# Kernel tuning notes

Hardware: AMD Instinct MI355X
Metric: run time of the kernel (lower is better)

Reference implementation:

```python
import jax, jax.numpy as jnp
import numpy as np

B, N, F_, H, K_IN, K = 2, 768, 128, 128, 2, 2
TAU = 0.66


def setup_inputs() -> dict:
    key = jax.random.key(0)
    ks = jax.random.split(key, 8)
    s = lambda fan: 1.0 / np.sqrt(fan)
    X = jax.random.normal(ks[0], (B, N, F_), jnp.float32)
    # edge_feat RezeroMLP: Linear(F,H) -> act -> Linear(H,H)
    ef_w1 = jax.random.normal(ks[1], (F_, H), jnp.float32) * s(F_)
    ef_b1 = jnp.zeros((H,), jnp.float32)
    ef_w2 = jax.random.normal(ks[2], (H, H), jnp.float32) * s(H)
    ef_b2 = jnp.zeros((H,), jnp.float32)
    # rezero gate (init 0 in module; use small nonzero so the branch is exercised)
    gate = jnp.asarray(0.1, jnp.float32)
    # score_mlp RezeroMLP: Linear(k_in,H) -> ReLU -> Linear(H,k)
    sm_w1 = jax.random.normal(ks[3], (K_IN, H), jnp.float32) * s(K_IN)
    sm_b1 = jnp.zeros((H,), jnp.float32)
    sm_w2 = jax.random.normal(ks[4], (H, K), jnp.float32) * s(H)
    sm_b2 = jnp.zeros((K,), jnp.float32)
    # pre-sampled standard Gumbel noise for gumbel_softmax
    u = jax.random.uniform(ks[5], (B, N, N, K), jnp.float32, minval=1e-6, maxval=1.0 - 1e-6)
    gumbel = -jnp.log(-jnp.log(u))
    return {"X": X, "ef_w1": ef_w1, "ef_b1": ef_b1, "ef_w2": ef_w2, "ef_b2": ef_b2,
            "gate": gate, "sm_w1": sm_w1, "sm_b1": sm_b1, "sm_w2": sm_w2, "sm_b2": sm_b2,
            "gumbel": gumbel}


def reference(X, ef_w1, ef_b1, ef_w2, ef_b2, gate, sm_w1, sm_b1, sm_w2, sm_b2, gumbel):
    # edge_feat MLP: [B,N,F] -> [B,N,H]
    feats = jax.nn.relu(X @ ef_w1 + ef_b1) @ ef_w2 + ef_b2
    D = H // K_IN
    Xact = feats.reshape(B, N, D, K_IN)
    Xskip = X.reshape(B, N, D, K_IN)  # feat_dim == hidden_dim, proj is None
    Xc = (Xskip + gate * Xact).transpose(0, 3, 1, 2)  # [B,k_in,N,D]
    # pairwise outer product ('prod' scoring): [B,N,N,k_in]
    prod = jnp.einsum('bkid,bkjd->bijk', Xc, Xc)
    # per-edge score MLP: k_in -> H -> k
    scores = jax.nn.relu(prod @ sm_w1 + sm_b1) @ sm_w2 + sm_b2  # [B,N,N,k]
    logits = scores - jnp.max(scores, axis=-1, keepdims=True)
    # gumbel-softmax, hard (straight-through)
    y_soft = jax.nn.softmax((logits + gumbel) / TAU, axis=-1)
    y_hard = jax.nn.one_hot(jnp.argmax(y_soft, axis=-1), K, dtype=y_soft.dtype)
    y = y_hard + y_soft - jax.lax.stop_gradient(y_soft)
    # A = y @ zo with zo = [0,1,...]: probability/one-hot mass of 'edge' states
    zo = jnp.ones((K,), y.dtype).at[0].set(0.0)
    A = y @ zo  # [B,N,N]
    # zero diagonal and symmetrize via upper triangle
    Au = jnp.triu(A, 1)
    return Au + jnp.swapaxes(Au, -1, -2)
```

## Files before the change

### kernel.cpp

```cpp
#include <hip/hip_runtime.h>

#define BB 2
#define NN 768
#define FF 128
#define HH 128
#define TS 32
#define LST 68
#define NT (NN / TS)
#define NPAIR (NT * (NT + 1) / 2)
#define EROWS 2
#define THR 4e-3f

__device__ __forceinline__
double edge_exact_f64(const double* __restrict__ Xc, const double* __restrict__ wpack,
                      int b, int i, int j, double init) {
    const double* xi0 = Xc + ((size_t)(b * 2 + 0) * NN + i) * 64;
    const double* xj0 = Xc + ((size_t)(b * 2 + 0) * NN + j) * 64;
    const double* xi1 = Xc + ((size_t)(b * 2 + 1) * NN + i) * 64;
    const double* xj1 = Xc + ((size_t)(b * 2 + 1) * NN + j) * 64;
    double p0 = 0.0, p1 = 0.0;
#pragma unroll 4
    for (int d2 = 0; d2 < 32; ++d2) {
        double2 a0 = *(const double2*)&xi0[2 * d2];
        double2 b0 = *(const double2*)&xj0[2 * d2];
        double2 a1 = *(const double2*)&xi1[2 * d2];
        double2 b1 = *(const double2*)&xj1[2 * d2];
        p0 = fma(a0.y, b0.y, fma(a0.x, b0.x, p0));
        p1 = fma(a1.y, b1.y, fma(a1.x, b1.x, p1));
    }
    double m = init;
#pragma unroll 8
    for (int c = 0; c < HH; ++c) {
        double2 wab = *(const double2*)&wpack[4 * c];
        double2 wbw = *(const double2*)&wpack[4 * c + 2];
        double tt = fma(p1, wab.y, fma(p0, wab.x, wbw.x));
        tt = fmax(tt, 0.0);
        m = fma(tt, wbw.y, m);
    }
    return m;
}

__global__ __launch_bounds__(128)
void edgefeat_kernel(const float* __restrict__ X,
                     const float* __restrict__ w1, const float* __restrict__ b1,
                     const float* __restrict__ w2, const float* __restrict__ b2,
                     const float* __restrict__ gatep,
                     const float* __restrict__ sm_w1, const float* __restrict__ sm_b1,
                     const float* __restrict__ sm_w2,
                     double* __restrict__ Xc, float* __restrict__ Xcf,
                     double* __restrict__ wpack, float4* __restrict__ wpackf) {
    __shared__ float  Xs[EROWS][FF];
    __shared__ double Hs[EROWS][HH];
    const int h = threadIdx.x;
    const int row0 = blockIdx.x * EROWS;
    for (int r = 0; r < EROWS; ++r) Xs[r][h] = X[(size_t)(row0 + r) * FF + h];
    if (blockIdx.x == 0) {
        double a  = (double)sm_w1[h];
        double bq = (double)sm_w1[HH + h];
        double be = (double)sm_b1[h];
        double wd = (double)sm_w2[2 * h + 1] - (double)sm_w2[2 * h + 0];
        wpack[4 * h + 0] = a;  wpack[4 * h + 1] = bq;
        wpack[4 * h + 2] = be; wpack[4 * h + 3] = wd;
        wpackf[h] = make_float4((float)a, (float)bq, (float)be, (float)wd);
    }
    __syncthreads();
    double acc[EROWS];
    double bb = (double)b1[h];
    for (int r = 0; r < EROWS; ++r) acc[r] = bb;
    for (int f = 0; f < FF; ++f) {
        double w = (double)w1[f * HH + h];
        for (int r = 0; r < EROWS; ++r) acc[r] = fma((double)Xs[r][f], w, acc[r]);
    }
    for (int r = 0; r < EROWS; ++r) Hs[r][h] = acc[r] > 0.0 ? acc[r] : 0.0;
    __syncthreads();
    bb = (double)b2[h];
    for (int r = 0; r < EROWS; ++r) acc[r] = bb;
    for (int c = 0; c < HH; ++c) {
        double w = (double)w2[c * HH + h];
        for (int r = 0; r < EROWS; ++r) acc[r] = fma(Hs[r][c], w, acc[r]);
    }
    const double gate = (double)gatep[0];
    const int k = h & 1, d = h >> 1;
    const int b = row0 / NN;
    const int i0 = row0 % NN;
    for (int r = 0; r < EROWS; ++r) {
        double v = (double)Xs[r][h] + gate * acc[r];
        size_t idx = (((size_t)(b * 2 + k)) * NN + (i0 + r)) * 64 + d;
        Xc[idx]  = v;
        Xcf[idx] = (float)v;
    }
}

__global__ __launch_bounds__(512, 6)
void edge_decide_kernel(const double* __restrict__ Xc,
                        const float* __restrict__ Xcf,
                        const double* __restrict__ wpack,
                        const float4* __restrict__ wpackf,
                        const float* __restrict__ sm_b2,
                        const float* __restrict__ gumbel,
                        float* __restrict__ out) {
    __shared__ float  Ai[2][TS][LST];
    __shared__ float  Aj[2][TS][LST];
    __shared__ float4 Wl[HH];
    __shared__ float  As[TS][TS + 1];
    const int b = blockIdx.y;
    const int t = blockIdx.x;
    int ti = (int)((49.0 - sqrt(2401.0 - 8.0 * (double)t)) * 0.5);
    int base = ti * (49 - ti) / 2;
    if (t < base) { --ti; base = ti * (49 - ti) / 2; }
    else { int nb = (ti + 1) * (48 - ti) / 2; if (t >= nb) { ++ti; base = nb; } }
    const int tj = t - base + ti;
    const int tid = threadIdx.x;
    const int i0 = ti * TS, j0 = tj * TS;

    for (int q = 0; q < 4; ++q) {
        int flat = tid + 512 * q;
        int dp = flat & 31;
        int r  = (flat >> 5) & 31;
        int k  = flat >> 10;
        size_t rowbase = ((size_t)(b * 2 + k)) * NN;
        *(float2*)&Ai[k][r][2 * dp] = *(const float2*)&Xcf[(rowbase + i0 + r) * 64 + 2 * dp];
        *(float2*)&Aj[k][r][2 * dp] = *(const float2*)&Xcf[(rowbase + j0 + r) * 64 + 2 * dp];
    }
    if (tid < HH) Wl[tid] = wpackf[tid];

    const int s  = tid & 1;
    const int e  = tid >> 1;
    const int rh = e >> 4;
    const int ch = e & 15;
    const int r0 = rh, r1 = rh + 16;
    const int c0 = 2 * ch, c1 = c0 + 1;
    const int gi0 = i0 + r0, gi1 = i0 + r1;
    const int gj0 = j0 + c0, gj1 = j0 + c1;

    float4 g0v = make_float4(0.f, 0.f, 0.f, 0.f);
    float4 g1v = make_float4(0.f, 0.f, 0.f, 0.f);
    if (s == 0) {
        g0v = *(const float4*)&gumbel[(((size_t)b * NN + gi0) * NN + gj0) * 2];
        g1v = *(const float4*)&gumbel[(((size_t)b * NN + gi1) * NN + gj0) * 2];
    }
    __syncthreads();

    float p000 = 0.f, p001 = 0.f, p010 = 0.f, p011 = 0.f;
    float p100 = 0.f, p101 = 0.f, p110 = 0.f, p111 = 0.f;
#pragma unroll
    for (int it = 0; it < 8; ++it) {
        const int d4 = (s + 2 * it) * 4;
        float4 a00 = *(const float4*)&Ai[0][r0][d4];
        float4 a01 = *(const float4*)&Ai[0][r1][d4];
        float4 a10 = *(const float4*)&Ai[1][r0][d4];
        float4 a11 = *(const float4*)&Ai[1][r1][d4];
        float4 b00 = *(const float4*)&Aj[0][c0][d4];
        float4 b01 = *(const float4*)&Aj[0][c1][d4];
        float4 b10 = *(const float4*)&Aj[1][c0][d4];
        float4 b11 = *(const float4*)&Aj[1][c1][d4];
        p000 = fmaf(a00.w, b00.w, fmaf(a00.z, b00.z, fmaf(a00.y, b00.y, fmaf(a00.x, b00.x, p000))));
        p001 = fmaf(a00.w, b01.w, fmaf(a00.z, b01.z, fmaf(a00.y, b01.y, fmaf(a00.x, b01.x, p001))));
        p010 = fmaf(a01.w, b00.w, fmaf(a01.z, b00.z, fmaf(a01.y, b00.y, fmaf(a01.x, b00.x, p010))));
        p011 = fmaf(a01.w, b01.w, fmaf(a01.z, b01.z, fmaf(a01.y, b01.y, fmaf(a01.x, b01.x, p011))));
        p100 = fmaf(a10.w, b10.w, fmaf(a10.z, b10.z, fmaf(a10.y, b10.y, fmaf(a10.x, b10.x, p100))));
        p101 = fmaf(a10.w, b11.w, fmaf(a10.z, b11.z, fmaf(a10.y, b11.y, fmaf(a10.x, b11.x, p101))));
        p110 = fmaf(a11.w, b10.w, fmaf(a11.z, b10.z, fmaf(a11.y, b10.y, fmaf(a11.x, b10.x, p110))));
        p111 = fmaf(a11.w, b11.w, fmaf(a11.z, b11.z, fmaf(a11.y, b11.y, fmaf(a11.x, b11.x, p111))));
    }
    p000 += __shfl_xor(p000, 1); p001 += __shfl_xor(p001, 1);
    p010 += __shfl_xor(p010, 1); p011 += __shfl_xor(p011, 1);
    p100 += __shfl_xor(p100, 1); p101 += __shfl_xor(p101, 1);
    p110 += __shfl_xor(p110, 1); p111 += __shfl_xor(p111, 1);

    float m00 = 0.f, m01 = 0.f, m10 = 0.f, m11 = 0.f;
#pragma unroll 8
    for (int it = 0; it < 64; ++it) {
        float4 w = Wl[s + 2 * it];
        float tt;
        tt = fmaf(p100, w.y, fmaf(p000, w.x, w.z)); tt = fmaxf(tt, 0.f); m00 = fmaf(tt, w.w, m00);
        tt = fmaf(p101, w.y, fmaf(p001, w.x, w.z)); tt = fmaxf(tt, 0.f); m01 = fmaf(tt, w.w, m01);
        tt = fmaf(p110, w.y, fmaf(p010, w.x, w.z)); tt = fmaxf(tt, 0.f); m10 = fmaf(tt, w.w, m10);
        tt = fmaf(p111, w.y, fmaf(p011, w.x, w.z)); tt = fmaxf(tt, 0.f); m11 = fmaf(tt, w.w, m11);
    }
    m00 += __shfl_xor(m00, 1); m01 += __shfl_xor(m01, 1);
    m10 += __shfl_xor(m10, 1); m11 += __shfl_xor(m11, 1);

    if (s == 0) {
        const double bd = (double)sm_b2[1] - (double)sm_b2[0];
        double i00 = bd + ((double)g0v.y - (double)g0v.x);
        double i01 = bd + ((double)g0v.w - (double)g0v.z);
        double i10 = bd + ((double)g1v.y - (double)g1v.x);
        double i11 = bd + ((double)g1v.w - (double)g1v.z);
        float f00 = m00 + (float)i00;
        float f01 = m01 + (float)i01;
        float f10 = m10 + (float)i10;
        float f11 = m11 + (float)i11;
        float A00 = f00 > 0.f ? 1.f : 0.f;
        float A01 = f01 > 0.f ? 1.f : 0.f;
        float A10 = f10 > 0.f ? 1.f : 0.f;
        float A11 = f11 > 0.f ? 1.f : 0.f;
        float fm = fminf(fminf(fabsf(f00), fabsf(f01)), fminf(fabsf(f10), fabsf(f11)));
        if (__builtin_expect(fm < THR, 0)) {
            if (fabsf(f00) < THR) A00 = edge_exact_f64(Xc, wpack, b, gi0, gj0, i00) > 0.0 ? 1.f : 0.f;
            if (fabsf(f01) < THR) A01 = edge_exact_f64(Xc, wpack, b, gi0, gj1, i01) > 0.0 ? 1.f : 0.f;
            if (fabsf(f10) < THR) A10 = edge_exact_f64(Xc, wpack, b, gi1, gj0, i10) > 0.0 ? 1.f : 0.f;
            if (fabsf(f11) < THR) A11 = edge_exact_f64(Xc, wpack, b, gi1, gj1, i11) > 0.0 ? 1.f : 0.f;
        }
        As[r0][c0] = A00; As[r0][c1] = A01;
        As[r1][c0] = A10; As[r1][c1] = A11;
    }
    __syncthreads();

    if (s == 0) {
        float A00 = As[r0][c0], A01 = As[r0][c1];
        float A10 = As[r1][c0], A11 = As[r1][c1];
        if (ti != tj) {
            *(float2*)&out[((size_t)b * NN + gi0) * NN + gj0] = make_float2(A00, A01);
            *(float2*)&out[((size_t)b * NN + gi1) * NN + gj0] = make_float2(A10, A11);
            float2 t0 = make_float2(As[c0][r0], As[c1][r0]);
            *(float2*)&out[((size_t)b * NN + j0 + r0) * NN + i0 + c0] = t0;
            float2 t1 = make_float2(As[c0][r1], As[c1][r1]);
            *(float2*)&out[((size_t)b * NN + j0 + r1) * NN + i0 + c0] = t1;
        } else {
            float v00 = (r0 < c0) ? A00 : ((r0 > c0) ? As[c0][r0] : 0.0f);
            float v01 = (r0 < c1) ? A01 : ((r0 > c1) ? As[c1][r0] : 0.0f);
            float v10 = (r1 < c0) ? A10 : ((r1 > c0) ? As[c0][r1] : 0.0f);
            float v11 = (r1 < c1) ? A11 : ((r1 > c1) ? As[c1][r1] : 0.0f);
            *(float2*)&out[((size_t)b * NN + gi0) * NN + gj0] = make_float2(v00, v01);
            *(float2*)&out[((size_t)b * NN + gi1) * NN + gj0] = make_float2(v10, v11);
        }
    }
}

extern "C" void kernel_launch(void* const* d_in, const int* in_sizes, int n_in,
                              void* d_out, int out_size, void* d_ws, size_t ws_size,
                              hipStream_t stream) {
    const float* X      = (const float*)d_in[0];
    const float* ef_w1  = (const float*)d_in[1];
    const float* ef_b1  = (const float*)d_in[2];
    const float* ef_w2  = (const float*)d_in[3];
    const float* ef_b2  = (const float*)d_in[4];
    const float* gate   = (const float*)d_in[5];
    const float* sm_w1  = (const float*)d_in[6];
    const float* sm_b1  = (const float*)d_in[7];
    const float* sm_w2  = (const float*)d_in[8];
    const float* sm_b2  = (const float*)d_in[9];
    const float* gumbel = (const float*)d_in[10];
    float* out = (float*)d_out;

    double* Xc     = (double*)d_ws;
    double* wpack  = Xc + (size_t)BB * 2 * NN * 64;
    float4* wpackf = (float4*)(wpack + 4 * HH);
    float*  Xcf    = (float*)(wpackf + HH);

    edgefeat_kernel<<<BB * NN / EROWS, 128, 0, stream>>>(
        X, ef_w1, ef_b1, ef_w2, ef_b2, gate, sm_w1, sm_b1, sm_w2, Xc, Xcf, wpack, wpackf);
    dim3 grid(NPAIR, BB);
    edge_decide_kernel<<<grid, 512, 0, stream>>>(Xc, Xcf, wpack, wpackf, sm_b2, gumbel, out);
}
```

Before: 119.1 us.

## Split score MLP by edge row across thread pair instead of by hidden unit

Before, the two threads of a pair each ran half of the 128 hidden units for all four edges, then reduced with shuffles, and only one of them did the gumbel, decision and output work. Now each thread runs all 128 hidden units for two edges (one row each), which removes the cross-lane reduction and the idle half-warp during the epilogue and stores. Weights are read straight from global/constant memory in chunks of eight instead of being staged in shared memory. This spreads the epilogue, gumbel loads and output stores over both threads, at the cost of more per-thread weight loads that depend on cache hits.

```diff
diff --git a/kernel.cpp b/kernel.cpp
--- a/kernel.cpp
+++ b/kernel.cpp
@@ -101,7 +101,6 @@
                         float* __restrict__ out) {
     __shared__ float  Ai[2][TS][LST];
     __shared__ float  Aj[2][TS][LST];
-    __shared__ float4 Wl[HH];
     __shared__ float  As[TS][TS + 1];
     const int b = blockIdx.y;
     const int t = blockIdx.x;
@@ -122,7 +121,6 @@
         *(float2*)&Ai[k][r][2 * dp] = *(const float2*)&Xcf[(rowbase + i0 + r) * 64 + 2 * dp];
         *(float2*)&Aj[k][r][2 * dp] = *(const float2*)&Xcf[(rowbase + j0 + r) * 64 + 2 * dp];
     }
-    if (tid < HH) Wl[tid] = wpackf[tid];
 
     const int s  = tid & 1;
     const int e  = tid >> 1;
@@ -130,15 +128,11 @@
     const int ch = e & 15;
     const int r0 = rh, r1 = rh + 16;
     const int c0 = 2 * ch, c1 = c0 + 1;
-    const int gi0 = i0 + r0, gi1 = i0 + r1;
+    const int lr  = (s == 0) ? r0 : r1;
+    const int gr  = i0 + lr;
     const int gj0 = j0 + c0, gj1 = j0 + c1;
 
-    float4 g0v = make_float4(0.f, 0.f, 0.f, 0.f);
-    float4 g1v = make_float4(0.f, 0.f, 0.f, 0.f);
-    if (s == 0) {
-        g0v = *(const float4*)&gumbel[(((size_t)b * NN + gi0) * NN + gj0) * 2];
-        g1v = *(const float4*)&gumbel[(((size_t)b * NN + gi1) * NN + gj0) * 2];
-    }
+    float4 gv = *(const float4*)&gumbel[(((size_t)b * NN + gr) * NN + gj0) * 2];
     __syncthreads();
 
     float p000 = 0.f, p001 = 0.f, p010 = 0.f, p011 = 0.f;
@@ -168,63 +162,47 @@
     p100 += __shfl_xor(p100, 1); p101 += __shfl_xor(p101, 1);
     p110 += __shfl_xor(p110, 1); p111 += __shfl_xor(p111, 1);
 
-    float m00 = 0.f, m01 = 0.f, m10 = 0.f, m11 = 0.f;
-#pragma unroll 8
-    for (int it = 0; it < 64; ++it) {
-        float4 w = Wl[s + 2 * it];
-        float tt;
-        tt = fmaf(p100, w.y, fmaf(p000, w.x, w.z)); tt = fmaxf(tt, 0.f); m00 = fmaf(tt, w.w, m00);
-        tt = fmaf(p101, w.y, fmaf(p001, w.x, w.z)); tt = fmaxf(tt, 0.f); m01 = fmaf(tt, w.w, m01);
-        tt = fmaf(p110, w.y, fmaf(p010, w.x, w.z)); tt = fmaxf(tt, 0.f); m10 = fmaf(tt, w.w, m10);
-        tt = fmaf(p111, w.y, fmaf(p011, w.x, w.z)); tt = fmaxf(tt, 0.f); m11 = fmaf(tt, w.w, m11);
-    }
-    m00 += __shfl_xor(m00, 1); m01 += __shfl_xor(m01, 1);
-    m10 += __shfl_xor(m10, 1); m11 += __shfl_xor(m11, 1);
-
-    if (s == 0) {
-        const double bd = (double)sm_b2[1] - (double)sm_b2[0];
-        double i00 = bd + ((double)g0v.y - (double)g0v.x);
-        double i01 = bd + ((double)g0v.w - (double)g0v.z);
-        double i10 = bd + ((double)g1v.y - (double)g1v.x);
-        double i11 = bd + ((double)g1v.w - (double)g1v.z);
-        float f00 = m00 + (float)i00;
-        float f01 = m01 + (float)i01;
-        float f10 = m10 + (float)i10;
-        float f11 = m11 + (float)i11;
-        float A00 = f00 > 0.f ? 1.f : 0.f;
-        float A01 = f01 > 0.f ? 1.f : 0.f;
-        float A10 = f10 > 0.f ? 1.f : 0.f;
-        float A11 = f11 > 0.f ? 1.f : 0.f;
-        float fm = fminf(fminf(fabsf(f00), fabsf(f01)), fminf(fabsf(f10), fabsf(f11)));
-        if (__builtin_expect(fm < THR, 0)) {
-            if (fabsf(f00) < THR) A00 = edge_exact_f64(Xc, wpack, b, gi0, gj0, i00) > 0.0 ? 1.f : 0.f;
-            if (fabsf(f01) < THR) A01 = edge_exact_f64(Xc, wpack, b, gi0, gj1, i01) > 0.0 ? 1.f : 0.f;
-            if (fabsf(f10) < THR) A10 = edge_exact_f64(Xc, wpack, b, gi1, gj0, i10) > 0.0 ? 1.f : 0.f;
-            if (fabsf(f11) < THR) A11 = edge_exact_f64(Xc, wpack, b, gi1, gj1, i11) > 0.0 ? 1.f : 0.f;
+    const float pa0 = (s == 0) ? p000 : p010;
+    const float pa1 = (s == 0) ? p100 : p110;
+    const float pb0 = (s == 0) ? p001 : p011;
+    const float pb1 = (s == 0) ? p101 : p111;
+
+    float ma = 0.f, mb = 0.f;
+#pragma unroll 1
+    for (int c = 0; c < HH; c += 8) {
+        float4 w[8];
+#pragma unroll
+        for (int u = 0; u < 8; ++u) w[u] = wpackf[c + u];
+#pragma unroll
+        for (int u = 0; u < 8; ++u) {
+            float tt;
+            tt = fmaf(pa1, w[u].y, fmaf(pa0, w[u].x, w[u].z)); tt = fmaxf(tt, 0.f); ma = fmaf(tt, w[u].w, ma);
+            tt = fmaf(pb1, w[u].y, fmaf(pb0, w[u].x, w[u].z)); tt = fmaxf(tt, 0.f); mb = fmaf(tt, w[u].w, mb);
         }
-        As[r0][c0] = A00; As[r0][c1] = A01;
-        As[r1][c0] = A10; As[r1][c1] = A11;
-    }
-    __syncthreads();
-
-    if (s == 0) {
-        float A00 = As[r0][c0], A01 = As[r0][c1];
-        float A10 = As[r1][c0], A11 = As[r1][c1];
-        if (ti != tj) {
-            *(float2*)&out[((size_t)b * NN + gi0) * NN + gj0] = make_float2(A00, A01);
-            *(float2*)&out[((size_t)b * NN + gi1) * NN + gj0] = make_float2(A10, A11);
-            float2 t0 = make_float2(As[c0][r0], As[c1][r0]);
-            *(float2*)&out[((size_t)b * NN + j0 + r0) * NN + i0 + c0] = t0;
-            float2 t1 = make_float2(As[c0][r1], As[c1][r1]);
-            *(float2*)&out[((size_t)b * NN + j0 + r1) * NN + i0 + c0] = t1;
-        } else {
-            float v00 = (r0 < c0) ? A00 : ((r0 > c0) ? As[c0][r0] : 0.0f);
-            float v01 = (r0 < c1) ? A01 : ((r0 > c1) ? As[c1][r0] : 0.0f);
-            float v10 = (r1 < c0) ? A10 : ((r1 > c0) ? As[c0][r1] : 0.0f);
-            float v11 = (r1 < c1) ? A11 : ((r1 > c1) ? As[c1][r1] : 0.0f);
-            *(float2*)&out[((size_t)b * NN + gi0) * NN + gj0] = make_float2(v00, v01);
-            *(float2*)&out[((size_t)b * NN + gi1) * NN + gj0] = make_float2(v10, v11);
-        }
+    }
+
+    const double bd = (double)sm_b2[1] - (double)sm_b2[0];
+    double ia = bd + ((double)gv.y - (double)gv.x);
+    double ib = bd + ((double)gv.w - (double)gv.z);
+    float fa = ma + (float)ia;
+    float fb = mb + (float)ib;
+    float Aa = fa > 0.f ? 1.f : 0.f;
+    float Ab = fb > 0.f ? 1.f : 0.f;
+    if (__builtin_expect(fminf(fabsf(fa), fabsf(fb)) < THR, 0)) {
+        if (fabsf(fa) < THR) Aa = edge_exact_f64(Xc, wpack, b, gr, gj0, ia) > 0.0 ? 1.f : 0.f;
+        if (fabsf(fb) < THR) Ab = edge_exact_f64(Xc, wpack, b, gr, gj1, ib) > 0.0 ? 1.f : 0.f;
+    }
+    As[lr][c0] = Aa; As[lr][c1] = Ab;
+    __syncthreads();
+
+    if (ti != tj) {
+        *(float2*)&out[((size_t)b * NN + gr) * NN + gj0] = make_float2(Aa, Ab);
+        float2 tv = make_float2(As[c0][lr], As[c1][lr]);
+        *(float2*)&out[((size_t)b * NN + j0 + lr) * NN + i0 + c0] = tv;
+    } else {
+        float v0 = (lr < c0) ? Aa : ((lr > c0) ? As[c0][lr] : 0.0f);
+        float v1 = (lr < c1) ? Ab : ((lr > c1) ? As[c1][lr] : 0.0f);
+        *(float2*)&out[((size_t)b * NN + gr) * NN + gj0] = make_float2(v0, v1);
     }
 }
 
```

Result: no change. 118.7 us (-0.4%).
